# Performance work log

Measured on AMD Instinct MI355X. Metric: run time of the kernel, lower is better.

## Reference

```python
import jax, jax.numpy as jnp
import numpy as np

N = 50000      # nodes
E = 800000     # edges
IN = 128       # in_channels
H = 128        # hidden_channels
OUT = 500      # out_channels
EPS = 1e-5


def setup_inputs() -> dict:
    key = jax.random.key(0)
    ks = jax.random.split(key, 8)
    def rn(k, shape, scale=0.05):
        return jax.random.normal(k, shape, jnp.float32) * scale
    return {
        "x": jax.random.normal(ks[0], (N, IN), jnp.float32),
        "edge_index": jax.random.randint(ks[1], (2, E), 0, N, dtype=jnp.int32),
        "W1": rn(ks[2], (IN, H)), "b1": jnp.zeros((H,), jnp.float32),
        "g1": jnp.ones((H,), jnp.float32), "be1": jnp.zeros((H,), jnp.float32),
        "W2": rn(ks[3], (H, 2 * H)), "b2": jnp.zeros((2 * H,), jnp.float32),
        "g2": jnp.ones((2 * H,), jnp.float32), "be2": jnp.zeros((2 * H,), jnp.float32),
        "W3": rn(ks[4], (2 * H, H)), "b3": jnp.zeros((H,), jnp.float32),
        "g3": jnp.ones((H,), jnp.float32), "be3": jnp.zeros((H,), jnp.float32),
        "Wl1": rn(ks[5], (H, H // 2)), "bl1": jnp.zeros((H // 2,), jnp.float32),
        "g4": jnp.ones((H // 2,), jnp.float32), "be4": jnp.zeros((H // 2,), jnp.float32),
        "Wl2": rn(ks[6], (H // 2, OUT)), "bl2": jnp.zeros((OUT,), jnp.float32),
    }


def layer_norm(x, g, b):
    mu = jnp.mean(x, axis=-1, keepdims=True)
    var = jnp.mean(jnp.square(x - mu), axis=-1, keepdims=True)
    return (x - mu) * jax.lax.rsqrt(var + EPS) * g + b


def gcn_conv(x, W, b, src, dst, n):
    # PyG GCNConv: x' = D^{-1/2} (A + I) D^{-1/2} (x W) + b, with self-loops.
    h = x @ W                                   # [N, F]
    ones = jnp.ones(src.shape[0], h.dtype)
    deg = jax.ops.segment_sum(ones, dst, num_segments=n) + 1.0  # +1 self-loop
    dinv = jnp.where(deg > 0, jax.lax.rsqrt(deg), 0.0)          # [N]
    coef = dinv[src] * dinv[dst]                # [E]
    agg = jax.ops.segment_sum(h[src] * coef[:, None], dst, num_segments=n)
    agg = agg + h * jnp.square(dinv)[:, None]   # self-loop messages
    return agg + b


def reference(x, edge_index, W1, b1, g1, be1, W2, b2, g2, be2,
              W3, b3, g3, be3, Wl1, bl1, g4, be4, Wl2, bl2):
    # eval mode: dropout is identity
    src, dst = edge_index[0], edge_index[1]
    n = x.shape[0]
    h = jax.nn.elu(layer_norm(gcn_conv(x, W1, b1, src, dst, n), g1, be1))
    h = jax.nn.elu(layer_norm(gcn_conv(h, W2, b2, src, dst, n), g2, be2))
    h = jax.nn.elu(layer_norm(gcn_conv(h, W3, b3, src, dst, n), g3, be3))
    h = jax.nn.elu(layer_norm(h @ Wl1 + bl1, g4, be4))
    return h @ Wl2 + bl2
```

## Files before the change

### kernel.cpp

```cpp
#include <hip/hip_runtime.h>
#include <cstdint>


#define LN_EPS 1e-5f

typedef __attribute__((ext_vector_type(8))) short bf16x8;
typedef __attribute__((ext_vector_type(4))) float f32x4;

static __device__ __forceinline__ ushort f2bf(float f) {
  union { float f; uint u; } c; c.f = f;
  uint u = c.u;
  return (ushort)((u + 0x7fffu + ((u >> 16) & 1u)) >> 16);
}
static __device__ __forceinline__ float bf2f(ushort h) {
  union { uint u; float f; } c; c.u = (uint)h << 16;
  return c.f;
}


__global__ void deg_kernel(const int* __restrict__ dst, int* __restrict__ deg, int E) {
  int e = blockIdx.x * blockDim.x + threadIdx.x;
  if (e < E) atomicAdd(&deg[dst[e]], 1);
}

__global__ void scan1_kernel(const int* __restrict__ deg, int* __restrict__ excl,
                             int* __restrict__ bsums, float* __restrict__ dinv, int N) {
  __shared__ int s[256];
  int tid = threadIdx.x;
  int i = blockIdx.x * 256 + tid;
  int v = (i < N) ? deg[i] : 0;
  s[tid] = v;
  __syncthreads();
  for (int o = 1; o < 256; o <<= 1) {
    int t = (tid >= o) ? s[tid - o] : 0;
    __syncthreads();
    if (tid >= o) s[tid] += t;
    __syncthreads();
  }
  if (i < N) {
    excl[i] = s[tid] - v;
    dinv[i] = rsqrtf((float)v + 1.0f);
  }
  if (tid == 255) bsums[blockIdx.x] = s[tid];
}

__global__ void scan23_kernel(int* __restrict__ rowptr, int* __restrict__ fill,
                              const int* __restrict__ bsums, int N, int Etotal, int nb) {
  __shared__ int sh[256];
  const int tid = threadIdx.x;
  const int bix = blockIdx.x;
  int v = (tid < bix && tid < nb) ? bsums[tid] : 0;
  sh[tid] = v;
  __syncthreads();
  for (int o = 128; o > 0; o >>= 1) {
    if (tid < o) sh[tid] += sh[tid + o];
    __syncthreads();
  }
  const int off = sh[0];
  int i = bix * 256 + tid;
  if (i < N) {
    int r = rowptr[i] + off;
    rowptr[i] = r;
    fill[i] = r;
  } else if (i == N) {
    rowptr[N] = Etotal;
  }
}

__global__ void fill_kernel(const int* __restrict__ src, const int* __restrict__ dst,
                            int* __restrict__ fill, int* __restrict__ srcs, int E) {
  int e = blockIdx.x * blockDim.x + threadIdx.x;
  if (e >= E) return;
  int idx = atomicAdd(&fill[dst[e]], 1);
  srcs[idx] = src[e];
}


struct WConvArgs {
  const float* w[5];
  ushort* wt[5];
  int K[5], N[5];
  int off[6];
};

__global__ void prep_kernel(WConvArgs a, int total, int* __restrict__ deg, int Nn) {
  int i = blockIdx.x * blockDim.x + threadIdx.x;
  if (i < Nn) deg[i] = 0;
  if (i < 768) a.wt[4][32000 + i] = 0;
  if (i >= total) return;
  int m = 0;
  while (i >= a.off[m + 1]) m++;
  int j = i - a.off[m];
  int k = j / a.N[m], n = j - k * a.N[m];
  a.wt[m][(size_t)n * a.K[m] + k] = f2bf(a.w[m][j]);
}

#define TBM 128
#define TBN 128
#define TBK 32
#define LDK 40

template <int AF32>
__global__ __launch_bounds__(256, 2) void mfma_gemm_kernel(
    const void* __restrict__ A, const ushort* __restrict__ Bt,
    const float* __restrict__ bias, ushort* __restrict__ Cout,
    int M, int N, int K) {
  __shared__ ushort As[TBM][LDK];
  __shared__ ushort Bs[TBN][LDK];
  const int tid = threadIdx.x;
  const int lane = tid & 63;
  const int w = tid >> 6;
  const int wm = w & 1, wn = w >> 1;
  const int quad = lane >> 4, l16 = lane & 15;
  const int rowBase = blockIdx.y * TBM;
  const int colBase = blockIdx.x * TBN;

  f32x4 acc[4][4] = {};
  const int lr = tid >> 2;
  const int lk = (tid & 3) * 8;

  for (int k0 = 0; k0 < K; k0 += TBK) {
#pragma unroll
    for (int h = 0; h < 2; h++) {
      int r = lr + h * 64;
      int grow = rowBase + r;
      if (AF32) {
        const float* Af = (const float*)A;
        float4 v0 = make_float4(0.f, 0.f, 0.f, 0.f), v1 = v0;
        if (grow < M) {
          const float* ap = Af + (size_t)grow * K + k0 + lk;
          v0 = *(const float4*)ap;
          v1 = *(const float4*)(ap + 4);
        }
        uint4 wv;
        wv.x = (uint)f2bf(v0.x) | ((uint)f2bf(v0.y) << 16);
        wv.y = (uint)f2bf(v0.z) | ((uint)f2bf(v0.w) << 16);
        wv.z = (uint)f2bf(v1.x) | ((uint)f2bf(v1.y) << 16);
        wv.w = (uint)f2bf(v1.z) | ((uint)f2bf(v1.w) << 16);
        *(uint4*)&As[r][lk] = wv;
      } else {
        const ushort* Ab = (const ushort*)A;
        uint4 va = make_uint4(0, 0, 0, 0);
        if (grow < M) va = *(const uint4*)(Ab + (size_t)grow * K + k0 + lk);
        *(uint4*)&As[r][lk] = va;
      }
      int gcol = colBase + r;
      uint4 vb = make_uint4(0, 0, 0, 0);
      if (gcol < N) vb = *(const uint4*)(Bt + (size_t)gcol * K + k0 + lk);
      *(uint4*)&Bs[r][lk] = vb;
    }
    __syncthreads();
    bf16x8 af[4], bfr[4];
#pragma unroll
    for (int i = 0; i < 4; i++) {
      af[i]  = *(const bf16x8*)&As[wm * 64 + i * 16 + l16][quad * 8];
      bfr[i] = *(const bf16x8*)&Bs[wn * 64 + i * 16 + l16][quad * 8];
    }
#pragma unroll
    for (int i = 0; i < 4; i++)
#pragma unroll
      for (int j = 0; j < 4; j++)
        acc[i][j] = __builtin_amdgcn_mfma_f32_16x16x32_bf16(af[i], bfr[j], acc[i][j], 0, 0, 0);
    __syncthreads();
  }
#pragma unroll
  for (int i = 0; i < 4; i++) {
    int row0 = rowBase + wm * 64 + i * 16 + quad * 4;
#pragma unroll
    for (int j = 0; j < 4; j++) {
      int col = colBase + wn * 64 + j * 16 + l16;
      if (col >= N) continue;
      float bv = bias ? bias[col] : 0.f;
#pragma unroll
      for (int r = 0; r < 4; r++) {
        int row = row0 + r;
        if (row >= M) continue;
        Cout[(size_t)row * N + col] = f2bf(acc[i][j][r] + bv);
      }
    }
  }
}


static __device__ __forceinline__ void acc8(float* a, uint4 v, float c) {
  a[0] += c * bf2f((ushort)(v.x & 0xffffu)); a[1] += c * bf2f((ushort)(v.x >> 16));
  a[2] += c * bf2f((ushort)(v.y & 0xffffu)); a[3] += c * bf2f((ushort)(v.y >> 16));
  a[4] += c * bf2f((ushort)(v.z & 0xffffu)); a[5] += c * bf2f((ushort)(v.z >> 16));
  a[6] += c * bf2f((ushort)(v.w & 0xffffu)); a[7] += c * bf2f((ushort)(v.w >> 16));
}

__global__ __launch_bounds__(512) void l2_kernel(
    const ushort* __restrict__ Hin, const int* __restrict__ rowptr,
    const int* __restrict__ srcs, const float* __restrict__ dinv,
    const ushort* __restrict__ W2t, const float* __restrict__ bias,
    const float* __restrict__ gamma, const float* __restrict__ beta,
    ushort* __restrict__ Hout, int M) {
  __shared__ ushort As[128][136];
  const int tid = threadIdx.x;
  const int lane = tid & 63;
  const int w = tid >> 6;
  const int g = lane >> 4, l16 = lane & 15;
  const int rowBase = blockIdx.x * 128;

  const uint4* h4 = (const uint4*)Hin;
  for (int it = 0; it < 16; ++it) {
    const int lrow = it * 8 + w;
    const int n = rowBase + lrow;
    if (n < M) {
      const float di = dinv[n];
      float a[8] = {0.f, 0.f, 0.f, 0.f, 0.f, 0.f, 0.f, 0.f};
      if (g == 0) {
        uint4 sv = h4[(size_t)n * 16 + l16];
        acc8(a, sv, di * di);
      }
      int i = rowptr[n] + g;
      const int e = rowptr[n + 1];
      for (; i + 4 < e; i += 8) {
        int s0 = srcs[i], s1 = srcs[i + 4];
        float c0 = dinv[s0] * di, c1 = dinv[s1] * di;
        uint4 v0 = h4[(size_t)s0 * 16 + l16];
        uint4 v1 = h4[(size_t)s1 * 16 + l16];
        acc8(a, v0, c0);
        acc8(a, v1, c1);
      }
      if (i < e) {
        int s = srcs[i];
        float c = dinv[s] * di;
        uint4 v = h4[(size_t)s * 16 + l16];
        acc8(a, v, c);
      }
#pragma unroll
      for (int k = 0; k < 8; k++) {
        a[k] += __shfl_xor(a[k], 16);
        a[k] += __shfl_xor(a[k], 32);
      }
      if (g == 0) {
        uint4 o;
        o.x = (uint)f2bf(a[0]) | ((uint)f2bf(a[1]) << 16);
        o.y = (uint)f2bf(a[2]) | ((uint)f2bf(a[3]) << 16);
        o.z = (uint)f2bf(a[4]) | ((uint)f2bf(a[5]) << 16);
        o.w = (uint)f2bf(a[6]) | ((uint)f2bf(a[7]) << 16);
        *(uint4*)&As[lrow][l16 * 8] = o;
      }
    }
  }
  __syncthreads();

  const int quad = g;
  const int wrow = w * 16;
  f32x4 acc[16] = {};
#pragma unroll
  for (int k0 = 0; k0 < 128; k0 += 32) {
    bf16x8 af = *(const bf16x8*)&As[wrow + l16][k0 + quad * 8];
#pragma unroll
    for (int j = 0; j < 16; j++) {
      bf16x8 bf = *(const bf16x8*)(W2t + (size_t)(j * 16 + l16) * 128 + k0 + quad * 8);
      acc[j] = __builtin_amdgcn_mfma_f32_16x16x32_bf16(af, bf, acc[j], 0, 0, 0);
    }
  }

#pragma unroll
  for (int r = 0; r < 4; r++) {
    float v[16];
    float s = 0.f;
#pragma unroll
    for (int j = 0; j < 16; j++) {
      v[j] = acc[j][r] + bias[j * 16 + l16];
      s += v[j];
    }
#pragma unroll
    for (int o = 8; o >= 1; o >>= 1) s += __shfl_xor(s, o, 16);
    float mean = s * (1.0f / 256.0f);
    float q = 0.f;
#pragma unroll
    for (int j = 0; j < 16; j++) {
      float d = v[j] - mean;
      q += d * d;
    }
#pragma unroll
    for (int o = 8; o >= 1; o >>= 1) q += __shfl_xor(q, o, 16);
    float rstd = rsqrtf(q * (1.0f / 256.0f) + LN_EPS);
    int grow = rowBase + wrow + quad * 4 + r;
    if (grow < M) {
#pragma unroll
      for (int j = 0; j < 16; j++) {
        int col = j * 16 + l16;
        float y = (v[j] - mean) * rstd * gamma[col] + beta[col];
        y = (y > 0.f) ? y : expm1f(y);
        Hout[(size_t)grow * 256 + col] = f2bf(y);
      }
    }
  }
}

__global__ __launch_bounds__(256) void l45_kernel(
    const ushort* __restrict__ A, const ushort* __restrict__ Bt1,
    const float* __restrict__ bias1, const float* __restrict__ gamma,
    const float* __restrict__ beta, const ushort* __restrict__ Bt2,
    const float* __restrict__ bias2, float* __restrict__ Cout, int M) {
  __shared__ ushort h4s[64][68];
  __shared__ __align__(16) float sout[16][500];
  const int tid = threadIdx.x;
  const int lane = tid & 63;
  const int w = tid >> 6;
  const int quad = lane >> 4, l16 = lane & 15;
  const int rowBase = blockIdx.x * 64;
  const int waveRow = rowBase + w * 16;

  bf16x8 bfr1[4][4];
#pragma unroll
  for (int j = 0; j < 4; j++)
#pragma unroll
    for (int kk = 0; kk < 4; kk++)
      bfr1[j][kk] = *(const bf16x8*)(Bt1 + (size_t)(j * 16 + l16) * 128 + kk * 32 + quad * 8);

  const int arow = waveRow + l16;
  bf16x8 af[4] = {};
  if (arow < M) {
#pragma unroll
    for (int kk = 0; kk < 4; kk++)
      af[kk] = *(const bf16x8*)(A + (size_t)arow * 128 + kk * 32 + quad * 8);
  }

  f32x4 acc1[4] = {};
#pragma unroll
  for (int j = 0; j < 4; j++)
#pragma unroll
    for (int kk = 0; kk < 4; kk++)
      acc1[j] = __builtin_amdgcn_mfma_f32_16x16x32_bf16(af[kk], bfr1[j][kk], acc1[j], 0, 0, 0);

#pragma unroll
  for (int r = 0; r < 4; r++) {
    float v[4];
    float s = 0.f;
#pragma unroll
    for (int j = 0; j < 4; j++) {
      v[j] = acc1[j][r] + bias1[j * 16 + l16];
      s += v[j];
    }
#pragma unroll
    for (int o = 8; o >= 1; o >>= 1) s += __shfl_xor(s, o, 16);
    float mean = s * (1.0f / 64.0f);
    float q = 0.f;
#pragma unroll
    for (int j = 0; j < 4; j++) {
      float d = v[j] - mean;
      q += d * d;
    }
#pragma unroll
    for (int o = 8; o >= 1; o >>= 1) q += __shfl_xor(q, o, 16);
    float rstd = rsqrtf(q * (1.0f / 64.0f) + LN_EPS);
    int lrow = w * 16 + quad * 4 + r;
#pragma unroll
    for (int j = 0; j < 4; j++) {
      int col = j * 16 + l16;
      float y = (v[j] - mean) * rstd * gamma[col] + beta[col];
      y = (y > 0.f) ? y : expm1f(y);
      h4s[lrow][col] = f2bf(y);
    }
  }

  bf16x8 breg[8][2];
  float bvreg[8];
#pragma unroll
  for (int c = 0; c < 8; c++) {
    const int bcol = (w * 8 + c) * 16 + l16;
    breg[c][0] = *(const bf16x8*)(Bt2 + (size_t)bcol * 64 + quad * 8);
    breg[c][1] = *(const bf16x8*)(Bt2 + (size_t)bcol * 64 + 32 + quad * 8);
    bvreg[c] = (bcol < 500) ? bias2[bcol] : 0.f;
  }
  __syncthreads();

#pragma unroll 1
  for (int rt = 0; rt < 4; rt++) {
    bf16x8 a0 = *(const bf16x8*)&h4s[rt * 16 + l16][quad * 8];
    bf16x8 a1 = *(const bf16x8*)&h4s[rt * 16 + l16][quad * 8 + 32];
#pragma unroll
    for (int c = 0; c < 8; c++) {
      f32x4 pacc = {0.f, 0.f, 0.f, 0.f};
      pacc = __builtin_amdgcn_mfma_f32_16x16x32_bf16(a0, breg[c][0], pacc, 0, 0, 0);
      pacc = __builtin_amdgcn_mfma_f32_16x16x32_bf16(a1, breg[c][1], pacc, 0, 0, 0);
      const int col = (w * 8 + c) * 16 + l16;
      if (col < 500) {
#pragma unroll
        for (int r = 0; r < 4; r++)
          sout[quad * 4 + r][col] = pacc[r] + bvreg[c];
      }
    }
    __syncthreads();
#pragma unroll
    for (int k = 0; k < 8; k++) {
      int idx = k * 256 + tid;
      if (idx < 2000) {
        int r = idx / 125;
        int c4 = idx - r * 125;
        int grow = rowBase + rt * 16 + r;
        if (grow < M) {
          float4 v = *(float4*)&sout[r][c4 * 4];
          *(float4*)&Cout[(size_t)grow * 500 + c4 * 4] = v;
        }
      }
    }
    __syncthreads();
  }
}

__global__ __launch_bounds__(256) void agg_ln_kernel(
    const ushort* __restrict__ hb, const int* __restrict__ rowptr,
    const int* __restrict__ srcs, const float* __restrict__ dinv,
    const float* __restrict__ bias, const float* __restrict__ gamma,
    const float* __restrict__ beta, uint* __restrict__ out, int Nn) {
  const int wave = threadIdx.x >> 6;
  const int n = blockIdx.x * 4 + wave;
  if (n >= Nn) return;
  const int lane = threadIdx.x & 63;
  const int g = lane >> 4, l16 = lane & 15;
  const uint4* h4 = (const uint4*)hb;
  const float di = dinv[n];
  float a[8] = {0.f, 0.f, 0.f, 0.f, 0.f, 0.f, 0.f, 0.f};
  if (g == 0) {
    uint4 sv = h4[(size_t)n * 16 + l16];
    acc8(a, sv, di * di);
    float4 b0 = ((const float4*)bias)[l16 * 2];
    float4 b1 = ((const float4*)bias)[l16 * 2 + 1];
    a[0] += b0.x; a[1] += b0.y; a[2] += b0.z; a[3] += b0.w;
    a[4] += b1.x; a[5] += b1.y; a[6] += b1.z; a[7] += b1.w;
  }
  int i = rowptr[n] + g;
  const int e = rowptr[n + 1];
  for (; i + 4 < e; i += 8) {
    int s0 = srcs[i], s1 = srcs[i + 4];
    float c0 = dinv[s0] * di, c1 = dinv[s1] * di;
    uint4 v0 = h4[(size_t)s0 * 16 + l16];
    uint4 v1 = h4[(size_t)s1 * 16 + l16];
    acc8(a, v0, c0);
    acc8(a, v1, c1);
  }
  if (i < e) {
    int s = srcs[i];
    float c = dinv[s] * di;
    uint4 v = h4[(size_t)s * 16 + l16];
    acc8(a, v, c);
  }
#pragma unroll
  for (int k = 0; k < 8; k++) {
    a[k] += __shfl_xor(a[k], 16);
    a[k] += __shfl_xor(a[k], 32);
  }
  float s = ((a[0] + a[1]) + (a[2] + a[3])) + ((a[4] + a[5]) + (a[6] + a[7]));
  s += __shfl_xor(s, 8);
  s += __shfl_xor(s, 4);
  s += __shfl_xor(s, 2);
  s += __shfl_xor(s, 1);
  float mean = s * (1.0f / 128.0f);
  float q = 0.f;
#pragma unroll
  for (int k = 0; k < 8; k++) {
    float d = a[k] - mean;
    q += d * d;
  }
  q += __shfl_xor(q, 8);
  q += __shfl_xor(q, 4);
  q += __shfl_xor(q, 2);
  q += __shfl_xor(q, 1);
  float rstd = rsqrtf(q * (1.0f / 128.0f) + LN_EPS);
  if (g == 0) {
    float4 g0 = ((const float4*)gamma)[l16 * 2];
    float4 g1 = ((const float4*)gamma)[l16 * 2 + 1];
    float4 e0 = ((const float4*)beta)[l16 * 2];
    float4 e1 = ((const float4*)beta)[l16 * 2 + 1];
    float gv[8] = {g0.x, g0.y, g0.z, g0.w, g1.x, g1.y, g1.z, g1.w};
    float ev[8] = {e0.x, e0.y, e0.z, e0.w, e1.x, e1.y, e1.z, e1.w};
    float y[8];
#pragma unroll
    for (int k = 0; k < 8; k++) {
      float t = (a[k] - mean) * rstd * gv[k] + ev[k];
      y[k] = (t > 0.f) ? t : expm1f(t);
    }
    uint4 o;
    o.x = (uint)f2bf(y[0]) | ((uint)f2bf(y[1]) << 16);
    o.y = (uint)f2bf(y[2]) | ((uint)f2bf(y[3]) << 16);
    o.z = (uint)f2bf(y[4]) | ((uint)f2bf(y[5]) << 16);
    o.w = (uint)f2bf(y[6]) | ((uint)f2bf(y[7]) << 16);
    ((uint4*)out)[(size_t)n * 16 + l16] = o;
  }
}


extern "C" void kernel_launch(void* const* d_in, const int* in_sizes, int n_in,
                              void* d_out, int out_size, void* d_ws, size_t ws_size,
                              hipStream_t stream) {
  const float* x   = (const float*)d_in[0];
  const int*   ei  = (const int*)d_in[1];
  const float* W1  = (const float*)d_in[2];
  const float* b1  = (const float*)d_in[3];
  const float* g1  = (const float*)d_in[4];
  const float* be1 = (const float*)d_in[5];
  const float* W2  = (const float*)d_in[6];
  const float* b2  = (const float*)d_in[7];
  const float* g2  = (const float*)d_in[8];
  const float* be2 = (const float*)d_in[9];
  const float* W3  = (const float*)d_in[10];
  const float* b3  = (const float*)d_in[11];
  const float* g3  = (const float*)d_in[12];
  const float* be3 = (const float*)d_in[13];
  const float* Wl1 = (const float*)d_in[14];
  const float* bl1 = (const float*)d_in[15];
  const float* g4  = (const float*)d_in[16];
  const float* be4 = (const float*)d_in[17];
  const float* Wl2 = (const float*)d_in[18];
  const float* bl2 = (const float*)d_in[19];

  const int N = in_sizes[0] / 128;
  const int E = in_sizes[1] / 2;
  const int* esrc = ei;
  const int* edst = ei + E;

  char* p = (char*)d_ws;
  ushort* Pb = (ushort*)p;            p += (size_t)N * 256 * 2;
  ushort* Qb = (ushort*)p;            p += (size_t)N * 256 * 2;
  ushort* W1t = (ushort*)p;           p += 128 * 128 * 2;
  ushort* W2t = (ushort*)p;           p += 128 * 256 * 2;
  ushort* W3t = (ushort*)p;           p += 256 * 128 * 2;
  ushort* Wl1t = (ushort*)p;          p += 128 * 64 * 2;
  ushort* Wl2t = (ushort*)p;          p += 64 * 512 * 2;
  int*   srcs  = (int*)p;             p += (size_t)E * 4;
  int*   deg   = (int*)p;             p += (size_t)N * 4;
  float* dinv  = (float*)p;           p += (size_t)N * 4;
  int*   rowptr= (int*)p;             p += (size_t)(N + 2) * 4;
  int*   fill  = (int*)p;             p += (size_t)N * 4;
  int*   bsums = (int*)p;             p += 256 * 4;

  const int nb = (N + 255) / 256;
  const int eb = (E + 255) / 256;

  WConvArgs wa;
  wa.w[0] = W1;  wa.wt[0] = W1t;  wa.K[0] = 128; wa.N[0] = 128;
  wa.w[1] = W2;  wa.wt[1] = W2t;  wa.K[1] = 128; wa.N[1] = 256;
  wa.w[2] = W3;  wa.wt[2] = W3t;  wa.K[2] = 256; wa.N[2] = 128;
  wa.w[3] = Wl1; wa.wt[3] = Wl1t; wa.K[3] = 128; wa.N[3] = 64;
  wa.w[4] = Wl2; wa.wt[4] = Wl2t; wa.K[4] = 64;  wa.N[4] = 500;
  wa.off[0] = 0;
  for (int m = 0; m < 5; m++) wa.off[m + 1] = wa.off[m] + wa.K[m] * wa.N[m];
  int wtotal = wa.off[5];
  int ptotal = wtotal > N ? wtotal : N;
  prep_kernel<<<(ptotal + 255) / 256, 256, 0, stream>>>(wa, wtotal, deg, N);

  deg_kernel<<<eb, 256, 0, stream>>>(edst, deg, E);
  scan1_kernel<<<nb, 256, 0, stream>>>(deg, rowptr, bsums, dinv, N);
  scan23_kernel<<<(N + 256) / 256, 256, 0, stream>>>(rowptr, fill, bsums, N, E, nb);
  fill_kernel<<<eb, 256, 0, stream>>>(esrc, edst, fill, srcs, E);

  const int ab = (N + 3) / 4;
  auto grid_of = [&](int M, int Nn) {
    return dim3((Nn + TBN - 1) / TBN, (M + TBM - 1) / TBM);
  };

  mfma_gemm_kernel<1><<<grid_of(N, 128), 256, 0, stream>>>(
      x, W1t, nullptr, Pb, N, 128, 128);
  agg_ln_kernel<<<ab, 256, 0, stream>>>(Pb, rowptr, srcs, dinv, b1, g1, be1, (uint*)Qb, N);

  l2_kernel<<<dim3((N + 127) / 128), 512, 0, stream>>>(
      Qb, rowptr, srcs, dinv, W2t, b2, g2, be2, Pb, N);

  mfma_gemm_kernel<0><<<grid_of(N, 128), 256, 0, stream>>>(
      Pb, W3t, nullptr, Qb, N, 128, 256);
  agg_ln_kernel<<<ab, 256, 0, stream>>>(Qb, rowptr, srcs, dinv, b3, g3, be3, (uint*)Pb, N);

  l45_kernel<<<dim3((N + 63) / 64), 256, 0, stream>>>(
      Pb, Wl1t, bl1, g4, be4, Wl2t, bl2, (float*)d_out, N);
}
```

Before: 571.7 us.

## Split layer-2 fused aggregate+GEMM into separate aggregation and tiled GEMM+LN kernels

Replaces the single layer-2 kernel, which aggregated 128 rows per block into LDS and then ran an MFMA GEMM reading weights from global memory, with two kernels. The first is a standalone one-wave-per-node aggregation that writes a bf16 intermediate. The second is an LDS-tiled 64x256 GEMM with a LayerNorm+ELU epilogue that reduces across waves through shared memory. This aims to give the irregular gather full occupancy and to stage weights through LDS, at the cost of an extra global round trip for the aggregated activations and one more launch. Buffer assignments for the later layers are swapped to match.

```diff
diff --git a/kernel.cpp b/kernel.cpp
--- a/kernel.cpp
+++ b/kernel.cpp
@@ -181,113 +181,112 @@
   }
 }
 
-
-static __device__ __forceinline__ void acc8(float* a, uint4 v, float c) {
-  a[0] += c * bf2f((ushort)(v.x & 0xffffu)); a[1] += c * bf2f((ushort)(v.x >> 16));
-  a[2] += c * bf2f((ushort)(v.y & 0xffffu)); a[3] += c * bf2f((ushort)(v.y >> 16));
-  a[4] += c * bf2f((ushort)(v.z & 0xffffu)); a[5] += c * bf2f((ushort)(v.z >> 16));
-  a[6] += c * bf2f((ushort)(v.w & 0xffffu)); a[7] += c * bf2f((ushort)(v.w >> 16));
-}
-
-__global__ __launch_bounds__(512) void l2_kernel(
-    const ushort* __restrict__ Hin, const int* __restrict__ rowptr,
-    const int* __restrict__ srcs, const float* __restrict__ dinv,
-    const ushort* __restrict__ W2t, const float* __restrict__ bias,
-    const float* __restrict__ gamma, const float* __restrict__ beta,
-    ushort* __restrict__ Hout, int M) {
-  __shared__ ushort As[128][136];
+__global__ __launch_bounds__(256) void l2gemm_ln_kernel(
+    const ushort* __restrict__ A, const ushort* __restrict__ Bt,
+    const float* __restrict__ bias, const float* __restrict__ gamma,
+    const float* __restrict__ beta, ushort* __restrict__ Hout, int M) {
+  __shared__ ushort As[64][LDK];
+  __shared__ ushort Bs[256][LDK];
+  __shared__ float ps[64][4];
+  __shared__ float qs[64][4];
   const int tid = threadIdx.x;
   const int lane = tid & 63;
   const int w = tid >> 6;
-  const int g = lane >> 4, l16 = lane & 15;
-  const int rowBase = blockIdx.x * 128;
-
-  const uint4* h4 = (const uint4*)Hin;
-  for (int it = 0; it < 16; ++it) {
-    const int lrow = it * 8 + w;
-    const int n = rowBase + lrow;
-    if (n < M) {
-      const float di = dinv[n];
-      float a[8] = {0.f, 0.f, 0.f, 0.f, 0.f, 0.f, 0.f, 0.f};
-      if (g == 0) {
-        uint4 sv = h4[(size_t)n * 16 + l16];
-        acc8(a, sv, di * di);
+  const int quad = lane >> 4, l16 = lane & 15;
+  const int rowBase = blockIdx.x * 64;
+
+  f32x4 acc[4][4] = {};
+  const int lr = tid >> 2;
+  const int lk = (tid & 3) * 8;
+
+  for (int k0 = 0; k0 < 128; k0 += TBK) {
+    {
+      int grow = rowBase + lr;
+      uint4 va = make_uint4(0, 0, 0, 0);
+      if (grow < M) va = *(const uint4*)(A + (size_t)grow * 128 + k0 + lk);
+      *(uint4*)&As[lr][lk] = va;
+#pragma unroll
+      for (int h = 0; h < 4; h++) {
+        int r = lr + h * 64;
+        uint4 vb = *(const uint4*)(Bt + (size_t)r * 128 + k0 + lk);
+        *(uint4*)&Bs[r][lk] = vb;
       }
-      int i = rowptr[n] + g;
-      const int e = rowptr[n + 1];
-      for (; i + 4 < e; i += 8) {
-        int s0 = srcs[i], s1 = srcs[i + 4];
-        float c0 = dinv[s0] * di, c1 = dinv[s1] * di;
-        uint4 v0 = h4[(size_t)s0 * 16 + l16];
-        uint4 v1 = h4[(size_t)s1 * 16 + l16];
-        acc8(a, v0, c0);
-        acc8(a, v1, c1);
+    }
+    __syncthreads();
+    bf16x8 af[4], bfr[4];
+#pragma unroll
+    for (int i = 0; i < 4; i++) {
+      af[i]  = *(const bf16x8*)&As[i * 16 + l16][quad * 8];
+      bfr[i] = *(const bf16x8*)&Bs[w * 64 + i * 16 + l16][quad * 8];
+    }
+#pragma unroll
+    for (int i = 0; i < 4; i++)
+#pragma unroll
+      for (int j = 0; j < 4; j++)
+        acc[i][j] = __builtin_amdgcn_mfma_f32_16x16x32_bf16(af[i], bfr[j], acc[i][j], 0, 0, 0);
+    __syncthreads();
+  }
+
+#pragma unroll
+  for (int j = 0; j < 4; j++) {
+    float bv = bias[w * 64 + j * 16 + l16];
+#pragma unroll
+    for (int i = 0; i < 4; i++)
+#pragma unroll
+      for (int r = 0; r < 4; r++) acc[i][j][r] += bv;
+  }
+
+#pragma unroll
+  for (int i = 0; i < 4; i++) {
+#pragma unroll
+    for (int r = 0; r < 4; r++) {
+      float p = (acc[i][0][r] + acc[i][1][r]) + (acc[i][2][r] + acc[i][3][r]);
+#pragma unroll
+      for (int o = 8; o >= 1; o >>= 1) p += __shfl_xor(p, o, 16);
+      if (l16 == 0) ps[i * 16 + quad * 4 + r][w] = p;
+    }
+  }
+  __syncthreads();
+  float mean[4][4];
+#pragma unroll
+  for (int i = 0; i < 4; i++)
+#pragma unroll
+    for (int r = 0; r < 4; r++) {
+      int lrow = i * 16 + quad * 4 + r;
+      mean[i][r] = ((ps[lrow][0] + ps[lrow][1]) + (ps[lrow][2] + ps[lrow][3])) * (1.0f / 256.0f);
+    }
+#pragma unroll
+  for (int i = 0; i < 4; i++) {
+#pragma unroll
+    for (int r = 0; r < 4; r++) {
+      float q = 0.f;
+#pragma unroll
+      for (int j = 0; j < 4; j++) {
+        float d = acc[i][j][r] - mean[i][r];
+        q += d * d;
       }
-      if (i < e) {
-        int s = srcs[i];
-        float c = dinv[s] * di;
-        uint4 v = h4[(size_t)s * 16 + l16];
-        acc8(a, v, c);
-      }
-#pragma unroll
-      for (int k = 0; k < 8; k++) {
-        a[k] += __shfl_xor(a[k], 16);
-        a[k] += __shfl_xor(a[k], 32);
-      }
-      if (g == 0) {
-        uint4 o;
-        o.x = (uint)f2bf(a[0]) | ((uint)f2bf(a[1]) << 16);
-        o.y = (uint)f2bf(a[2]) | ((uint)f2bf(a[3]) << 16);
-        o.z = (uint)f2bf(a[4]) | ((uint)f2bf(a[5]) << 16);
-        o.w = (uint)f2bf(a[6]) | ((uint)f2bf(a[7]) << 16);
-        *(uint4*)&As[lrow][l16 * 8] = o;
-      }
+#pragma unroll
+      for (int o = 8; o >= 1; o >>= 1) q += __shfl_xor(q, o, 16);
+      if (l16 == 0) qs[i * 16 + quad * 4 + r][w] = q;
     }
   }
   __syncthreads();
-
-  const int quad = g;
-  const int wrow = w * 16;
-  f32x4 acc[16] = {};
-#pragma unroll
-  for (int k0 = 0; k0 < 128; k0 += 32) {
-    bf16x8 af = *(const bf16x8*)&As[wrow + l16][k0 + quad * 8];
-#pragma unroll
-    for (int j = 0; j < 16; j++) {
-      bf16x8 bf = *(const bf16x8*)(W2t + (size_t)(j * 16 + l16) * 128 + k0 + quad * 8);
-      acc[j] = __builtin_amdgcn_mfma_f32_16x16x32_bf16(af, bf, acc[j], 0, 0, 0);
-    }
-  }
-
-#pragma unroll
-  for (int r = 0; r < 4; r++) {
-    float v[16];
-    float s = 0.f;
-#pragma unroll
-    for (int j = 0; j < 16; j++) {
-      v[j] = acc[j][r] + bias[j * 16 + l16];
-      s += v[j];
-    }
-#pragma unroll
-    for (int o = 8; o >= 1; o >>= 1) s += __shfl_xor(s, o, 16);
-    float mean = s * (1.0f / 256.0f);
-    float q = 0.f;
-#pragma unroll
-    for (int j = 0; j < 16; j++) {
-      float d = v[j] - mean;
-      q += d * d;
-    }
-#pragma unroll
-    for (int o = 8; o >= 1; o >>= 1) q += __shfl_xor(q, o, 16);
-    float rstd = rsqrtf(q * (1.0f / 256.0f) + LN_EPS);
-    int grow = rowBase + wrow + quad * 4 + r;
-    if (grow < M) {
-#pragma unroll
-      for (int j = 0; j < 16; j++) {
-        int col = j * 16 + l16;
-        float y = (v[j] - mean) * rstd * gamma[col] + beta[col];
-        y = (y > 0.f) ? y : expm1f(y);
-        Hout[(size_t)grow * 256 + col] = f2bf(y);
+#pragma unroll
+  for (int i = 0; i < 4; i++) {
+#pragma unroll
+    for (int r = 0; r < 4; r++) {
+      int lrow = i * 16 + quad * 4 + r;
+      int grow = rowBase + lrow;
+      float var = ((qs[lrow][0] + qs[lrow][1]) + (qs[lrow][2] + qs[lrow][3])) * (1.0f / 256.0f);
+      float rstd = rsqrtf(var + LN_EPS);
+      if (grow < M) {
+#pragma unroll
+        for (int j = 0; j < 4; j++) {
+          int col = w * 64 + j * 16 + l16;
+          float y = (acc[i][j][r] - mean[i][r]) * rstd * gamma[col] + beta[col];
+          y = (y > 0.f) ? y : expm1f(y);
+          Hout[(size_t)grow * 256 + col] = f2bf(y);
+        }
       }
     }
   }
@@ -402,6 +401,61 @@
       }
     }
     __syncthreads();
+  }
+}
+
+
+static __device__ __forceinline__ void acc8(float* a, uint4 v, float c) {
+  a[0] += c * bf2f((ushort)(v.x & 0xffffu)); a[1] += c * bf2f((ushort)(v.x >> 16));
+  a[2] += c * bf2f((ushort)(v.y & 0xffffu)); a[3] += c * bf2f((ushort)(v.y >> 16));
+  a[4] += c * bf2f((ushort)(v.z & 0xffffu)); a[5] += c * bf2f((ushort)(v.z >> 16));
+  a[6] += c * bf2f((ushort)(v.w & 0xffffu)); a[7] += c * bf2f((ushort)(v.w >> 16));
+}
+
+__global__ __launch_bounds__(256) void agg_kernel(
+    const ushort* __restrict__ hb, const int* __restrict__ rowptr,
+    const int* __restrict__ srcs, const float* __restrict__ dinv,
+    uint* __restrict__ out, int Nn) {
+  const int wave = threadIdx.x >> 6;
+  const int n = blockIdx.x * 4 + wave;
+  if (n >= Nn) return;
+  const int lane = threadIdx.x & 63;
+  const int g = lane >> 4, l16 = lane & 15;
+  const uint4* h4 = (const uint4*)hb;
+  const float di = dinv[n];
+  float a[8] = {0.f, 0.f, 0.f, 0.f, 0.f, 0.f, 0.f, 0.f};
+  if (g == 0) {
+    uint4 sv = h4[(size_t)n * 16 + l16];
+    acc8(a, sv, di * di);
+  }
+  int i = rowptr[n] + g;
+  const int e = rowptr[n + 1];
+  for (; i + 4 < e; i += 8) {
+    int s0 = srcs[i], s1 = srcs[i + 4];
+    float c0 = dinv[s0] * di, c1 = dinv[s1] * di;
+    uint4 v0 = h4[(size_t)s0 * 16 + l16];
+    uint4 v1 = h4[(size_t)s1 * 16 + l16];
+    acc8(a, v0, c0);
+    acc8(a, v1, c1);
+  }
+  if (i < e) {
+    int s = srcs[i];
+    float c = dinv[s] * di;
+    uint4 v = h4[(size_t)s * 16 + l16];
+    acc8(a, v, c);
+  }
+#pragma unroll
+  for (int k = 0; k < 8; k++) {
+    a[k] += __shfl_xor(a[k], 16);
+    a[k] += __shfl_xor(a[k], 32);
+  }
+  if (g == 0) {
+    uint4 o;
+    o.x = (uint)f2bf(a[0]) | ((uint)f2bf(a[1]) << 16);
+    o.y = (uint)f2bf(a[2]) | ((uint)f2bf(a[3]) << 16);
+    o.z = (uint)f2bf(a[4]) | ((uint)f2bf(a[5]) << 16);
+    o.w = (uint)f2bf(a[6]) | ((uint)f2bf(a[7]) << 16);
+    ((uint4*)out)[(size_t)n * 16 + l16] = o;
   }
 }
 
@@ -560,13 +614,14 @@
       x, W1t, nullptr, Pb, N, 128, 128);
   agg_ln_kernel<<<ab, 256, 0, stream>>>(Pb, rowptr, srcs, dinv, b1, g1, be1, (uint*)Qb, N);
 
-  l2_kernel<<<dim3((N + 127) / 128), 512, 0, stream>>>(
-      Qb, rowptr, srcs, dinv, W2t, b2, g2, be2, Pb, N);
+  agg_kernel<<<ab, 256, 0, stream>>>(Qb, rowptr, srcs, dinv, (uint*)Pb, N);
+  l2gemm_ln_kernel<<<dim3((N + 63) / 64), 256, 0, stream>>>(
+      Pb, W2t, b2, g2, be2, Qb, N);
 
   mfma_gemm_kernel<0><<<grid_of(N, 128), 256, 0, stream>>>(
-      Pb, W3t, nullptr, Qb, N, 128, 256);
-  agg_ln_kernel<<<ab, 256, 0, stream>>>(Qb, rowptr, srcs, dinv, b3, g3, be3, (uint*)Pb, N);
+      Qb, W3t, nullptr, Pb, N, 128, 256);
+  agg_ln_kernel<<<ab, 256, 0, stream>>>(Pb, rowptr, srcs, dinv, b3, g3, be3, (uint*)Qb, N);
 
   l45_kernel<<<dim3((N + 63) / 64), 256, 0, stream>>>(
-      Pb, Wl1t, bl1, g4, be4, Wl2t, bl2, (float*)d_out, N);
-}
+      Qb, Wl1t, bl1, g4, be4, Wl2t, bl2, (float*)d_out, N);
+}
```

After: 482.5 us. 15.6% less time.
